# Performance work log

Measured on AMD Instinct MI355X. Metric: run time of the kernel, lower is better.

Reference implementation:

```python
import jax, jax.numpy as jnp
import numpy as np

N, E, B = 8000, 128000, 16
DIN, D, H, C, L = 16, 256, 8, 32, 6
MC, NT = 200, 8
NEG_SLOPE = 0.2


def layernorm(x, s, b):
    mu = jnp.mean(x, axis=-1, keepdims=True)
    var = jnp.mean(jnp.square(x - mu), axis=-1, keepdims=True)
    return (x - mu) * jax.lax.rsqrt(var + 1e-5) * s + b


def setup_inputs() -> dict:
    key = jax.random.key(0)
    ks = iter(jax.random.split(key, 64))
    rn = lambda shape, s=0.05: jax.random.normal(next(ks), shape, jnp.float32) * s
    inp = {}
    inp['x'] = jax.random.normal(next(ks), (N, DIN), jnp.float32)
    inp['edge_index'] = jax.random.randint(next(ks), (2, E), 0, N)
    inp['batch'] = jnp.sort(jax.random.randint(next(ks), (N,), 0, B))
    # node encoder: Linear(DIN,D) + LayerNorm
    inp['enc_W'] = rn((DIN, D)); inp['enc_b'] = jnp.zeros((D,), jnp.float32)
    inp['enc_ls'] = jnp.ones((D,), jnp.float32); inp['enc_lb'] = jnp.zeros((D,), jnp.float32)
    # GATv2 layers (stacked): lin_l, lin_r, att, output bias, post LayerNorm
    inp['Wl'] = rn((L, D, D)); inp['bl'] = jnp.zeros((L, D), jnp.float32)
    inp['Wr'] = rn((L, D, D)); inp['br'] = jnp.zeros((L, D), jnp.float32)
    inp['att'] = rn((L, H, C))
    inp['gb'] = jnp.zeros((L, D), jnp.float32)
    inp['gls'] = jnp.ones((L, D), jnp.float32); inp['glb'] = jnp.zeros((L, D), jnp.float32)
    # color head MLP: D -> D -> D//2 -> MC
    inp['cW1'] = rn((D, D)); inp['cb1'] = jnp.zeros((D,), jnp.float32)
    inp['cW2'] = rn((D, D // 2)); inp['cb2'] = jnp.zeros((D // 2,), jnp.float32)
    inp['cW3'] = rn((D // 2, MC)); inp['cb3'] = jnp.zeros((MC,), jnp.float32)
    # chromatic head: 2D -> D -> D//2 -> MC
    inp['chW1'] = rn((2 * D, D)); inp['chb1'] = jnp.zeros((D,), jnp.float32)
    inp['chW2'] = rn((D, D // 2)); inp['chb2'] = jnp.zeros((D // 2,), jnp.float32)
    inp['chW3'] = rn((D // 2, MC)); inp['chb3'] = jnp.zeros((MC,), jnp.float32)
    # type head: 2D -> 128 -> NT
    inp['tW1'] = rn((2 * D, 128)); inp['tb1'] = jnp.zeros((128,), jnp.float32)
    inp['tW2'] = rn((128, NT)); inp['tb2'] = jnp.zeros((NT,), jnp.float32)
    # difficulty head: 2D -> 64 -> 1, sigmoid * 100
    inp['dW1'] = rn((2 * D, 64)); inp['db1'] = jnp.zeros((64,), jnp.float32)
    inp['dW2'] = rn((64, 1)); inp['db2'] = jnp.zeros((1,), jnp.float32)
    return inp


def reference(x, edge_index, batch, enc_W, enc_b, enc_ls, enc_lb,
              Wl, bl, Wr, br, att, gb, gls, glb,
              cW1, cb1, cW2, cb2, cW3, cb3,
              chW1, chb1, chW2, chb2, chW3, chb3,
              tW1, tb1, tW2, tb2, dW1, db1, dW2, db2):
    n = x.shape[0]
    # node encoder (dropout = identity at inference)
    h = jax.nn.relu(layernorm(x @ enc_W + enc_b, enc_ls, enc_lb))
    # add self loops once (same for every layer)
    sl = jnp.arange(n)
    src = jnp.concatenate([edge_index[0], sl])  # message source j
    dst = jnp.concatenate([edge_index[1], sl])  # message target i
    for i in range(L):
        xl = (h @ Wl[i] + bl[i]).reshape(n, H, C)  # source transform
        xr = (h @ Wr[i] + br[i]).reshape(n, H, C)  # target transform
        # GATv2 attention: a^T LeakyReLU(xl_j + xr_i)
        e = jax.nn.leaky_relu(xl[src] + xr[dst], NEG_SLOPE)  # [E+N, H, C]
        logits = jnp.einsum('ehc,hc->eh', e, att[i])          # [E+N, H]
        # segment softmax over destination node (self-loops guarantee denom > 0)
        m = jax.ops.segment_max(logits, dst, num_segments=n)
        m = jnp.where(jnp.isfinite(m), m, 0.0)
        p = jnp.exp(logits - m[dst])
        denom = jax.ops.segment_sum(p, dst, num_segments=n)
        alpha = p / denom[dst]
        out = jax.ops.segment_sum(xl[src] * alpha[:, :, None], dst, num_segments=n)
        out = out.reshape(n, D) + gb[i]
        h_new = jax.nn.elu(layernorm(out, gls[i], glb[i]))
        h = h + h_new if i > 0 else h_new
    # per-node color logits
    z = jax.nn.relu(h @ cW1 + cb1)
    z = jax.nn.relu(z @ cW2 + cb2)
    node_colors = z @ cW3 + cb3
    # global mean/max pooling per graph
    cnt = jax.ops.segment_sum(jnp.ones((n,), h.dtype), batch, num_segments=B)
    mean_p = jax.ops.segment_sum(h, batch, num_segments=B) / jnp.maximum(cnt, 1.0)[:, None]
    max_p = jax.ops.segment_max(h, batch, num_segments=B)
    max_p = jnp.where(jnp.isfinite(max_p), max_p, 0.0)
    g = jnp.concatenate([mean_p, max_p], axis=1)  # [B, 2D]
    zc = jax.nn.relu(g @ chW1 + chb1)
    zc = jax.nn.relu(zc @ chW2 + chb2)
    chromatic_num = zc @ chW3 + chb3
    zt = jax.nn.relu(g @ tW1 + tb1)
    graph_type = zt @ tW2 + tb2
    zd = jax.nn.relu(g @ dW1 + db1)
    difficulty = jax.nn.sigmoid(zd @ dW2 + db2) * 100.0
    return (node_colors, chromatic_num, graph_type, difficulty)
```

## Files before the change

### kernel.cpp

```cpp
#include <hip/hip_runtime.h>
#include <hip/hip_bf16.h>

constexpr int DIN = 16;
constexpr int D   = 256;
constexpr int NH  = 8;
constexpr int NC  = 32;
constexpr int MC  = 200;
constexpr int NT  = 8;
constexpr int BG  = 16;
constexpr int NL  = 6;
constexpr float NEG = 0.2f;

typedef __attribute__((ext_vector_type(8))) short bfrag;
typedef __attribute__((ext_vector_type(4))) float f32x4;

__device__ inline unsigned short f2bf(float f) {
    unsigned int u = __float_as_uint(f);
    u += 0x7FFFu + ((u >> 16) & 1u);
    return (unsigned short)(u >> 16);
}
__device__ inline float bf2f(unsigned short u) {
    return __uint_as_float((unsigned int)u << 16);
}

__device__ inline float dot_ilp(const float* g, const float* __restrict__ W, int K, int ldw, int t) {
    float a0 = 0.f, a1 = 0.f, a2 = 0.f, a3 = 0.f;
    for (int k = 0; k < K; k += 4) {
        a0 = fmaf(g[k + 0], W[(k + 0) * ldw + t], a0);
        a1 = fmaf(g[k + 1], W[(k + 1) * ldw + t], a1);
        a2 = fmaf(g[k + 2], W[(k + 2) * ldw + t], a2);
        a3 = fmaf(g[k + 3], W[(k + 3) * ldw + t], a3);
    }
    return (a0 + a1) + (a2 + a3);
}


__device__ inline void enc_node(const float* x, const float* W, const float* b, const float* ls,
                                const float* lb, float* h, int n, int lane) {
    int c4 = lane * 4;
    float xs[DIN];
#pragma unroll
    for (int k = 0; k < DIN; k += 4) {
        float4 xv = *(const float4*)&x[n * DIN + k];
        xs[k] = xv.x; xs[k + 1] = xv.y; xs[k + 2] = xv.z; xs[k + 3] = xv.w;
    }
    float4 a = *(const float4*)&b[c4];
#pragma unroll
    for (int k = 0; k < DIN; k++) {
        float4 wv = *(const float4*)&W[k * D + c4];
        a.x = fmaf(xs[k], wv.x, a.x);
        a.y = fmaf(xs[k], wv.y, a.y);
        a.z = fmaf(xs[k], wv.z, a.z);
        a.w = fmaf(xs[k], wv.w, a.w);
    }
    float s = a.x + a.y + a.z + a.w;
#pragma unroll
    for (int msk = 1; msk <= 32; msk <<= 1) s += __shfl_xor(s, msk);
    float mu = s * (1.f / D);
    float4 dv = make_float4(a.x - mu, a.y - mu, a.z - mu, a.w - mu);
    float v2 = dv.x * dv.x + dv.y * dv.y + dv.z * dv.z + dv.w * dv.w;
#pragma unroll
    for (int msk = 1; msk <= 32; msk <<= 1) v2 += __shfl_xor(v2, msk);
    float rstd = rsqrtf(v2 * (1.f / D) + 1e-5f);
    float4 lsv = *(const float4*)&ls[c4];
    float4 lbv = *(const float4*)&lb[c4];
    float4 y = make_float4(fmaxf(dv.x * rstd * lsv.x + lbv.x, 0.f),
                           fmaxf(dv.y * rstd * lsv.y + lbv.y, 0.f),
                           fmaxf(dv.z * rstd * lsv.z + lbv.z, 0.f),
                           fmaxf(dv.w * rstd * lsv.w + lbv.w, 0.f));
    *(float4*)&h[(size_t)n * D + c4] = y;
}

__device__ inline float4 attn_compute(const unsigned short* xl, const unsigned short* xr,
                                      const int* row_ptr, const int* col, const float* att,
                                      const float* gb, const float* gls, const float* glb,
                                      const float* h, int layer, int n, int lane) {
    int c4 = lane * 4;
    ushort4 xr4 = *(const ushort4*)&xr[(size_t)n * D + c4];
    float4 xrv = make_float4(bf2f(xr4.x), bf2f(xr4.y), bf2f(xr4.z), bf2f(xr4.w));
    float4 av  = *(const float4*)&att[c4];
    int beg = row_ptr[n], end = row_ptr[n + 1];
    int deg = end - beg;
    int myc = col[beg + min(lane, deg - 1)];
    float l = 0.f;
    float4 acc = make_float4(0.f, 0.f, 0.f, 0.f);
    auto loadx = [&](int i) -> ushort4 {
        if (i < deg) {
            int s = (i < 64) ? __shfl(myc, i) : col[beg + i];
            return *(const ushort4*)&xl[(size_t)s * D + c4];
        }
        return make_ushort4(0, 0, 0, 0);
    };
    auto step = [&](ushort4 x4) {
        float4 xlv = make_float4(bf2f(x4.x), bf2f(x4.y), bf2f(x4.z), bf2f(x4.w));
        float sx = xlv.x + xrv.x; sx = sx > 0.f ? sx : NEG * sx;
        float sy = xlv.y + xrv.y; sy = sy > 0.f ? sy : NEG * sy;
        float sz = xlv.z + xrv.z; sz = sz > 0.f ? sz : NEG * sz;
        float sw = xlv.w + xrv.w; sw = sw > 0.f ? sw : NEG * sw;
        float z = av.x * sx + av.y * sy + av.z * sz + av.w * sw;
        z += __shfl_xor(z, 1); z += __shfl_xor(z, 2); z += __shfl_xor(z, 4);
        float p = __expf(z);
        l += p;
        acc.x = fmaf(p, xlv.x, acc.x);
        acc.y = fmaf(p, xlv.y, acc.y);
        acc.z = fmaf(p, xlv.z, acc.z);
        acc.w = fmaf(p, xlv.w, acc.w);
    };
    ushort4 b0 = loadx(0), b1 = loadx(1), b2 = loadx(2), b3 = loadx(3);
    int e = 0;
    for (; e + 4 <= deg; e += 4) {
        ushort4 n0 = loadx(e + 4), n1 = loadx(e + 5), n2 = loadx(e + 6), n3 = loadx(e + 7);
        step(b0); step(b1); step(b2); step(b3);
        b0 = n0; b1 = n1; b2 = n2; b3 = n3;
    }
    if (e + 0 < deg) step(b0);
    if (e + 1 < deg) step(b1);
    if (e + 2 < deg) step(b2);
    float4 gbv = *(const float4*)&gb[c4];
    float rl = 1.f / l;
    float4 o = make_float4(acc.x * rl + gbv.x, acc.y * rl + gbv.y,
                           acc.z * rl + gbv.z, acc.w * rl + gbv.w);
    float s = o.x + o.y + o.z + o.w;
#pragma unroll
    for (int msk = 1; msk <= 32; msk <<= 1) s += __shfl_xor(s, msk);
    float mu = s * (1.f / D);
    float4 dv = make_float4(o.x - mu, o.y - mu, o.z - mu, o.w - mu);
    float v2 = dv.x * dv.x + dv.y * dv.y + dv.z * dv.z + dv.w * dv.w;
#pragma unroll
    for (int msk = 1; msk <= 32; msk <<= 1) v2 += __shfl_xor(v2, msk);
    float rstd = rsqrtf(v2 * (1.f / D) + 1e-5f);
    float4 glsv = *(const float4*)&gls[c4];
    float4 glbv = *(const float4*)&glb[c4];
    float y0 = dv.x * rstd * glsv.x + glbv.x;
    float y1 = dv.y * rstd * glsv.y + glbv.y;
    float y2 = dv.z * rstd * glsv.z + glbv.z;
    float y3 = dv.w * rstd * glsv.w + glbv.w;
    y0 = y0 > 0.f ? y0 : expm1f(y0);
    y1 = y1 > 0.f ? y1 : expm1f(y1);
    y2 = y2 > 0.f ? y2 : expm1f(y2);
    y3 = y3 > 0.f ? y3 : expm1f(y3);
    float4 prev = make_float4(0.f, 0.f, 0.f, 0.f);
    if (layer > 0) prev = *(const float4*)&h[(size_t)n * D + c4];
    return make_float4(prev.x + y0, prev.y + y1, prev.z + y2, prev.w + y3);
}

__device__ inline void gemm_one_ct(const unsigned short (*As)[264],
                                   const unsigned short* WpL, const unsigned short* WpR,
                                   const float* bl, const float* br,
                                   unsigned short* xl, unsigned short* xr,
                                   int N, int nb, int ctg, int lane) {
    int m = lane & 15, q = lane >> 4;
    float bLv = bl[ctg * 16 + m];
    float bRv = br[ctg * 16 + m];
    f32x4 accL = (f32x4){bLv, bLv, bLv, bLv};
    f32x4 accR = (f32x4){bRv, bRv, bRv, bRv};
#pragma unroll
    for (int ks = 0; ks < 8; ks++) {
        bfrag af = *(const bfrag*)&As[m][ks * 32 + q * 8];
        size_t off = (((size_t)ctg * 8 + ks) * 64 + lane) * 8;
        bfrag bL = *(const bfrag*)&WpL[off];
        bfrag bR = *(const bfrag*)&WpR[off];
        accL = __builtin_amdgcn_mfma_f32_16x16x32_bf16(af, bL, accL, 0, 0, 0);
        accR = __builtin_amdgcn_mfma_f32_16x16x32_bf16(af, bR, accR, 0, 0, 0);
    }
    int colg = ctg * 16 + m;
#pragma unroll
    for (int reg = 0; reg < 4; reg++) {
        int row = nb + q * 4 + reg;
        if (row < N) {
            xl[(size_t)row * D + colg] = f2bf(accL[reg]);
            xr[(size_t)row * D + colg] = f2bf(accR[reg]);
        }
    }
}

__device__ inline void gemm_core(const unsigned short (*As)[264],
                                 const unsigned short* WpL, const unsigned short* WpR,
                                 const float* bl, const float* br,
                                 unsigned short* xl, unsigned short* xr, int N, int nb, int T) {
    int lane = T & 63, w = T >> 6;
#pragma unroll
    for (int ct = 0; ct < 4; ct++)
        gemm_one_ct(As, WpL, WpR, bl, br, xl, xr, N, nb, w * 4 + ct, lane);
}

__device__ inline void repack_attn_one(const float* Wl, const float* Wr, unsigned short* Wp, int tid) {
    int lane = tid & 63;
    int r1 = tid >> 6;
    int ks = r1 & 7;
    int r2 = r1 >> 3;
    int ct = r2 & 15;
    int mi = r2 >> 4;
    int layer = mi >> 1, mat = mi & 1;
    const float* W = (mat == 0 ? Wl : Wr) + (size_t)layer * D * D;
    int n = ct * 16 + (lane & 15);
    int kb = ks * 32 + (lane >> 4) * 8;
    size_t base = (((size_t)(mi * 16 + ct) * 8 + ks) * 64 + lane) * 8;
#pragma unroll
    for (int j = 0; j < 8; j++) Wp[base + j] = f2bf(W[(size_t)(kb + j) * D + n]);
}

__device__ inline void repack_gen_one(const float* W, unsigned short* Wp, int K, int NCOL, int nks, int tid) {
    int lane = tid & 63;
    int r = tid >> 6;
    int ks = r % nks;
    int ct = r / nks;
    int n = ct * 16 + (lane & 15);
    int kb = ks * 32 + (lane >> 4) * 8;
    size_t base = (((size_t)ct * nks + ks) * 64 + lane) * 8;
#pragma unroll
    for (int j = 0; j < 8; j++) {
        int k = kb + j;
        Wp[base + j] = (n < NCOL && k < K) ? f2bf(W[(size_t)k * NCOL + n]) : (unsigned short)0;
    }
}


__global__ __launch_bounds__(256) void fused_init_k(const float* __restrict__ x, const float* __restrict__ encW,
                                                    const float* __restrict__ encb, const float* __restrict__ encls,
                                                    const float* __restrict__ enclb, float* __restrict__ h, int N,
                                                    const int* __restrict__ dst, int* __restrict__ deg, int E,
                                                    const float* __restrict__ Wl, const float* __restrict__ Wr,
                                                    unsigned short* __restrict__ Wp,
                                                    const float* __restrict__ cW1, unsigned short* __restrict__ cW1p,
                                                    const float* __restrict__ cW2, unsigned short* __restrict__ cW2p,
                                                    const float* __restrict__ cW3, unsigned short* __restrict__ cW3p) {
    int gid = blockIdx.x * 256 + threadIdx.x;
    int lane = threadIdx.x & 63;
    int n = blockIdx.x * 4 + (threadIdx.x >> 6);
    if (n < N) enc_node(x, encW, encb, encls, enclb, h, n, lane);
    if (gid < E) atomicAdd(&deg[dst[gid]], 1);
    if (gid < NL * 2 * 16 * 8 * 64) repack_attn_one(Wl, Wr, Wp, gid);
    if (gid < 16 * 8 * 64) repack_gen_one(cW1, cW1p, D, D, 8, gid);
    if (gid < 8 * 8 * 64)  repack_gen_one(cW2, cW2p, D, 128, 8, gid);
    if (gid < 13 * 4 * 64) repack_gen_one(cW3, cW3p, 128, MC, 4, gid);
}

__global__ __launch_bounds__(1024) void scan_k(const int* __restrict__ deg, int* __restrict__ row_ptr,
                                               int* __restrict__ fill, int N) {
    __shared__ int sd[1024];
    int t = threadIdx.x;
    int chunk = (N + 1023) >> 10;
    int lo = t * chunk, hi = min(lo + chunk, N);
    int s = 0;
    for (int i = lo; i < hi; i++) s += deg[i] + 1;
    sd[t] = s;
    __syncthreads();
    for (int off = 1; off < 1024; off <<= 1) {
        int v = (t >= off) ? sd[t - off] : 0;
        __syncthreads();
        sd[t] += v;
        __syncthreads();
    }
    int run = (t > 0) ? sd[t - 1] : 0;
    for (int i = lo; i < hi; i++) {
        row_ptr[i] = run; fill[i] = run;
        run += deg[i] + 1;
    }
    if (t == 1023) row_ptr[N] = sd[1023];
}

__global__ __launch_bounds__(256) void scatter_gemm0_k(const int* __restrict__ src, const int* __restrict__ dst,
                                                       int* __restrict__ fill, int* __restrict__ col, int E, int N,
                                                       const float* __restrict__ h,
                                                       const unsigned short* __restrict__ WpL,
                                                       const unsigned short* __restrict__ WpR,
                                                       const float* __restrict__ bl, const float* __restrict__ br,
                                                       unsigned short* __restrict__ xl, unsigned short* __restrict__ xr) {
    __shared__ unsigned short As[16][264];
    int T = threadIdx.x;
    int tt = blockIdx.x;
    int ntiles = (N + 15) >> 4;
    if (tt < ntiles) {
        int nb = tt * 16;
#pragma unroll
        for (int r = 0; r < 16; r++) {
            int row = nb + r;
            float v = (row < N) ? h[(size_t)row * D + T] : 0.f;
            As[r][T] = f2bf(v);
        }
        __syncthreads();
        gemm_core(As, WpL, WpR, bl, br, xl, xr, N, nb, T);
    }
    for (int e = blockIdx.x * 256 + T; e < E + N; e += gridDim.x * 256) {
        if (e < E) {
            int p = atomicAdd(&fill[dst[e]], 1);
            col[p] = src[e];
        } else {
            int n = e - E;
            int p = atomicAdd(&fill[n], 1);
            col[p] = n;
        }
    }
}

__global__ __launch_bounds__(1024) void layer_k(const unsigned short* __restrict__ xl_in,
                                                const unsigned short* __restrict__ xr_in,
                                                const int* __restrict__ row_ptr, const int* __restrict__ col,
                                                const float* __restrict__ att, const float* __restrict__ gb,
                                                const float* __restrict__ gls, const float* __restrict__ glb,
                                                float* __restrict__ h, int layer, int N,
                                                const unsigned short* __restrict__ WpL,
                                                const unsigned short* __restrict__ WpR,
                                                const float* __restrict__ bl, const float* __restrict__ br,
                                                unsigned short* __restrict__ xl_out, unsigned short* __restrict__ xr_out) {
    __shared__ unsigned short As[16][264];
    int T = threadIdx.x;
    int lane = T & 63, wv = T >> 6;
    int nb = blockIdx.x * 16;
    int c4 = lane * 4;
    int n = nb + wv;
    if (n < N) {
        float4 r = attn_compute(xl_in, xr_in, row_ptr, col, att, gb, gls, glb, h, layer, n, lane);
        *(float4*)&h[(size_t)n * D + c4] = r;
        As[wv][c4 + 0] = f2bf(r.x);
        As[wv][c4 + 1] = f2bf(r.y);
        As[wv][c4 + 2] = f2bf(r.z);
        As[wv][c4 + 3] = f2bf(r.w);
    } else {
        As[wv][c4 + 0] = 0; As[wv][c4 + 1] = 0; As[wv][c4 + 2] = 0; As[wv][c4 + 3] = 0;
    }
    __syncthreads();
    gemm_one_ct((const unsigned short (*)[264])As, WpL, WpR, bl, br, xl_out, xr_out, N, nb, wv, lane);
}

__global__ __launch_bounds__(1024) void last_k(const unsigned short* __restrict__ xl_in,
                                               const unsigned short* __restrict__ xr_in,
                                               const int* __restrict__ row_ptr, const int* __restrict__ col,
                                               const float* __restrict__ att, const float* __restrict__ gb,
                                               const float* __restrict__ gls, const float* __restrict__ glb,
                                               float* __restrict__ h, int N,
                                               const unsigned short* __restrict__ W1p, const float* __restrict__ b1,
                                               const unsigned short* __restrict__ W2p, const float* __restrict__ b2,
                                               const unsigned short* __restrict__ W3p, const float* __restrict__ b3,
                                               float* __restrict__ out) {
    __shared__ unsigned short As[16][264];
    __shared__ unsigned short Zs[16][264];
    int T = threadIdx.x;
    int lane = T & 63, wv = T >> 6;
    int nb = blockIdx.x * 16;
    int c4 = lane * 4;
    int n = nb + wv;
    if (n < N) {
        float4 res = attn_compute(xl_in, xr_in, row_ptr, col, att, gb, gls, glb, h, NL - 1, n, lane);
        *(float4*)&h[(size_t)n * D + c4] = res;
        As[wv][c4 + 0] = f2bf(res.x);
        As[wv][c4 + 1] = f2bf(res.y);
        As[wv][c4 + 2] = f2bf(res.z);
        As[wv][c4 + 3] = f2bf(res.w);
    } else {
        As[wv][c4 + 0] = 0; As[wv][c4 + 1] = 0; As[wv][c4 + 2] = 0; As[wv][c4 + 3] = 0;
    }
    __syncthreads();
    int m = lane & 15, q = lane >> 4;
    {
        float bv = b1[wv * 16 + m];
        f32x4 acc = (f32x4){bv, bv, bv, bv};
#pragma unroll
        for (int ks = 0; ks < 8; ks++) {
            bfrag af = *(const bfrag*)&As[m][ks * 32 + q * 8];
            bfrag bf = *(const bfrag*)&W1p[(((size_t)wv * 8 + ks) * 64 + lane) * 8];
            acc = __builtin_amdgcn_mfma_f32_16x16x32_bf16(af, bf, acc, 0, 0, 0);
        }
        int colg = wv * 16 + m;
#pragma unroll
        for (int reg = 0; reg < 4; reg++)
            Zs[q * 4 + reg][colg] = f2bf(fmaxf(acc[reg], 0.f));
    }
    __syncthreads();
    if (wv < 8) {
        float bv = b2[wv * 16 + m];
        f32x4 acc = (f32x4){bv, bv, bv, bv};
#pragma unroll
        for (int ks = 0; ks < 8; ks++) {
            bfrag af = *(const bfrag*)&Zs[m][ks * 32 + q * 8];
            bfrag bf = *(const bfrag*)&W2p[(((size_t)wv * 8 + ks) * 64 + lane) * 8];
            acc = __builtin_amdgcn_mfma_f32_16x16x32_bf16(af, bf, acc, 0, 0, 0);
        }
        int colg = wv * 16 + m;
#pragma unroll
        for (int reg = 0; reg < 4; reg++)
            As[q * 4 + reg][colg] = f2bf(fmaxf(acc[reg], 0.f));
    }
    __syncthreads();
    if (wv < 13) {
        int colg = wv * 16 + m;
        float bv = (colg < MC) ? b3[colg] : 0.f;
        f32x4 acc = (f32x4){bv, bv, bv, bv};
#pragma unroll
        for (int ks = 0; ks < 4; ks++) {
            bfrag af = *(const bfrag*)&As[m][ks * 32 + q * 8];
            bfrag bf = *(const bfrag*)&W3p[(((size_t)wv * 4 + ks) * 64 + lane) * 8];
            acc = __builtin_amdgcn_mfma_f32_16x16x32_bf16(af, bf, acc, 0, 0, 0);
        }
#pragma unroll
        for (int reg = 0; reg < 4; reg++) {
            int row = nb + q * 4 + reg;
            if (row < N && colg < MC) out[(size_t)row * MC + colg] = acc[reg];
        }
    }
}

__global__ __launch_bounds__(1024) void poolheads_k(const float* __restrict__ h, const int* __restrict__ batch,
                                                    int N,
                                                    const float* __restrict__ chW1, const float* __restrict__ chb1,
                                                    const float* __restrict__ chW2, const float* __restrict__ chb2,
                                                    const float* __restrict__ chW3, const float* __restrict__ chb3,
                                                    const float* __restrict__ tW1, const float* __restrict__ tb1,
                                                    const float* __restrict__ tW2, const float* __restrict__ tb2,
                                                    const float* __restrict__ dW1, const float* __restrict__ db1,
                                                    const float* __restrict__ dW2, const float* __restrict__ db2,
                                                    float* __restrict__ out_ch, float* __restrict__ out_t,
                                                    float* __restrict__ out_d) {
    int b = blockIdx.x, t = threadIdx.x;
    int sl = t >> 8, c = t & 255;
    int lo = 0, hi = N;
    while (lo < hi) { int mid = (lo + hi) >> 1; if (batch[mid] < b) lo = mid + 1; else hi = mid; }
    int s0 = lo;
    lo = 0; hi = N;
    while (lo < hi) { int mid = (lo + hi) >> 1; if (batch[mid] < b + 1) lo = mid + 1; else hi = mid; }
    int s1 = lo;
    int len = s1 - s0;
    int chunk = (len + 3) >> 2;
    int n0 = s0 + sl * chunk;
    int n1 = min(n0 + chunk, s1);
    float sum = 0.f, mx = -3.0e38f;
    int n = n0;
    for (; n + 4 <= n1; n += 4) {
        float v0 = h[(size_t)(n + 0) * D + c];
        float v1 = h[(size_t)(n + 1) * D + c];
        float v2 = h[(size_t)(n + 2) * D + c];
        float v3 = h[(size_t)(n + 3) * D + c];
        sum += (v0 + v1) + (v2 + v3);
        mx = fmaxf(mx, fmaxf(fmaxf(v0, v1), fmaxf(v2, v3)));
    }
    for (; n < n1; n++) { float v = h[(size_t)n * D + c]; sum += v; mx = fmaxf(mx, v); }
    __shared__ float ps[4][256];
    __shared__ float pm[4][256];
    __shared__ float g[2 * D];
    __shared__ float z1[D];
    __shared__ float z2[128];
    ps[sl][c] = sum; pm[sl][c] = mx;
    __syncthreads();
    if (t < 256) {
        float s = (ps[0][t] + ps[1][t]) + (ps[2][t] + ps[3][t]);
        float m = fmaxf(fmaxf(pm[0][t], pm[1][t]), fmaxf(pm[2][t], pm[3][t]));
        g[t] = s / fmaxf((float)len, 1.f);
        g[D + t] = (len > 0) ? m : 0.f;
    }
    __syncthreads();
    if (t < 256) z1[t] = fmaxf(chb1[t] + dot_ilp(g, chW1, 2 * D, D, t), 0.f);
    __syncthreads();
    if (t < 128) z2[t] = fmaxf(chb2[t] + dot_ilp(z1, chW2, D, 128, t), 0.f);
    __syncthreads();
    if (t < MC) out_ch[b * MC + t] = chb3[t] + dot_ilp(z2, chW3, 128, MC, t);
    if (t < 128) z1[t] = fmaxf(tb1[t] + dot_ilp(g, tW1, 2 * D, 128, t), 0.f);
    __syncthreads();
    if (t < NT) out_t[b * NT + t] = tb2[t] + dot_ilp(z1, tW2, 128, NT, t);
    if (t < 64) z2[t] = fmaxf(db1[t] + dot_ilp(g, dW1, 2 * D, 64, t), 0.f);
    __syncthreads();
    if (t == 0) {
        float a = db2[0] + dot_ilp(z2, dW2, 64, 1, 0);
        out_d[b] = 100.f / (1.f + __expf(-a));
    }
}

extern "C" void kernel_launch(void* const* d_in, const int* in_sizes, int n_in,
                              void* d_out, int out_size, void* d_ws, size_t ws_size,
                              hipStream_t stream) {
    const float* x     = (const float*)d_in[0];
    const int*   ei    = (const int*)d_in[1];
    const int*   batch = (const int*)d_in[2];
    const float* encW  = (const float*)d_in[3];
    const float* encb  = (const float*)d_in[4];
    const float* encls = (const float*)d_in[5];
    const float* enclb = (const float*)d_in[6];
    const float* Wl    = (const float*)d_in[7];
    const float* bl    = (const float*)d_in[8];
    const float* Wr    = (const float*)d_in[9];
    const float* br    = (const float*)d_in[10];
    const float* att   = (const float*)d_in[11];
    const float* gb    = (const float*)d_in[12];
    const float* gls   = (const float*)d_in[13];
    const float* glb   = (const float*)d_in[14];
    const float* cW1   = (const float*)d_in[15];
    const float* cb1   = (const float*)d_in[16];
    const float* cW2   = (const float*)d_in[17];
    const float* cb2   = (const float*)d_in[18];
    const float* cW3   = (const float*)d_in[19];
    const float* cb3   = (const float*)d_in[20];
    const float* chW1  = (const float*)d_in[21];
    const float* chb1  = (const float*)d_in[22];
    const float* chW2  = (const float*)d_in[23];
    const float* chb2  = (const float*)d_in[24];
    const float* chW3  = (const float*)d_in[25];
    const float* chb3  = (const float*)d_in[26];
    const float* tW1   = (const float*)d_in[27];
    const float* tb1   = (const float*)d_in[28];
    const float* tW2   = (const float*)d_in[29];
    const float* tb2   = (const float*)d_in[30];
    const float* dW1   = (const float*)d_in[31];
    const float* db1   = (const float*)d_in[32];
    const float* dW2   = (const float*)d_in[33];
    const float* db2   = (const float*)d_in[34];

    const int N = in_sizes[0] / DIN;
    const int E = in_sizes[1] / 2;
    const int* esrc = ei;
    const int* edst = ei + E;

    char* p = (char*)d_ws;
    auto carve = [&](size_t bytes) { char* r = p; p += (bytes + 255) & ~(size_t)255; return r; };
    int*            row_ptr = (int*)carve((size_t)(N + 1) * 4);
    int*            fill    = (int*)carve((size_t)N * 4);
    int*            deg     = (int*)carve((size_t)N * 4);
    int*            col     = (int*)carve((size_t)(E + N) * 4);
    unsigned short* Wp      = (unsigned short*)carve((size_t)NL * 2 * 65536 * 2);
    unsigned short* cW1p    = (unsigned short*)carve((size_t)16 * 8 * 64 * 8 * 2);
    unsigned short* cW2p    = (unsigned short*)carve((size_t)8 * 8 * 64 * 8 * 2);
    unsigned short* cW3p    = (unsigned short*)carve((size_t)13 * 4 * 64 * 8 * 2);
    float*          h       = (float*)carve((size_t)N * D * 4);
    unsigned short* xlA     = (unsigned short*)carve((size_t)N * D * 2);
    unsigned short* xrA     = (unsigned short*)carve((size_t)N * D * 2);
    unsigned short* xlB     = (unsigned short*)carve((size_t)N * D * 2);
    unsigned short* xrB     = (unsigned short*)carve((size_t)N * D * 2);
    (void)ws_size; (void)n_in; (void)out_size;

    const int ntiles16 = (N + 15) / 16;
    const int sblocks  = max(ntiles16, (E + N + 255) / 256);
    const int fblocks  = max((N + 3) / 4, max((E + 255) / 256, 384));

    hipMemsetAsync(deg, 0, (size_t)N * 4, stream);
    fused_init_k<<<fblocks, 256, 0, stream>>>(x, encW, encb, encls, enclb, h, N,
                                              edst, deg, E, Wl, Wr, Wp,
                                              cW1, cW1p, cW2, cW2p, cW3, cW3p);
    scan_k<<<1, 1024, 0, stream>>>(deg, row_ptr, fill, N);
    scatter_gemm0_k<<<sblocks, 256, 0, stream>>>(esrc, edst, fill, col, E, N, h,
                                                 Wp + 0, Wp + (size_t)65536,
                                                 bl + 0, br + 0, xlA, xrA);
    for (int l = 0; l < NL - 1; l++) {
        const unsigned short* xin_l = (l & 1) ? xlB : xlA;
        const unsigned short* xin_r = (l & 1) ? xrB : xrA;
        unsigned short* xout_l = (l & 1) ? xlA : xlB;
        unsigned short* xout_r = (l & 1) ? xrA : xrB;
        layer_k<<<ntiles16, 1024, 0, stream>>>(xin_l, xin_r, row_ptr, col, att + l * NH * NC,
                                               gb + l * D, gls + l * D, glb + l * D, h, l, N,
                                               Wp + (size_t)((l + 1) * 2 + 0) * 65536,
                                               Wp + (size_t)((l + 1) * 2 + 1) * 65536,
                                               bl + (l + 1) * D, br + (l + 1) * D, xout_l, xout_r);
    }
    float* out = (float*)d_out;
    last_k<<<ntiles16, 1024, 0, stream>>>(xlB, xrB, row_ptr, col, att + (NL - 1) * NH * NC,
                                          gb + (NL - 1) * D, gls + (NL - 1) * D, glb + (NL - 1) * D, h, N,
                                          cW1p, cb1, cW2p, cb2, cW3p, cb3, out);
    poolheads_k<<<BG, 1024, 0, stream>>>(h, batch, N, chW1, chb1, chW2, chb2, chW3, chb3,
                                         tW1, tb1, tW2, tb2, dW1, db1, dW2, db2,
                                         out + (size_t)N * MC,
                                         out + (size_t)N * MC + BG * MC,
                                         out + (size_t)N * MC + BG * MC + BG * NT);
}
```

Before: 447.8 us.

## Split pooling and graph heads into separate wider-grid kernels

After: 425.3 us. 1.05x faster.

```diff
diff --git a/kernel.cpp b/kernel.cpp
--- a/kernel.cpp
+++ b/kernel.cpp
@@ -9,6 +9,7 @@
 constexpr int NT  = 8;
 constexpr int BG  = 16;
 constexpr int NL  = 6;
+constexpr int PS  = 16;
 constexpr float NEG = 0.2f;
 
 typedef __attribute__((ext_vector_type(8))) short bfrag;
@@ -401,19 +402,12 @@
     }
 }
 
-__global__ __launch_bounds__(1024) void poolheads_k(const float* __restrict__ h, const int* __restrict__ batch,
-                                                    int N,
-                                                    const float* __restrict__ chW1, const float* __restrict__ chb1,
-                                                    const float* __restrict__ chW2, const float* __restrict__ chb2,
-                                                    const float* __restrict__ chW3, const float* __restrict__ chb3,
-                                                    const float* __restrict__ tW1, const float* __restrict__ tb1,
-                                                    const float* __restrict__ tW2, const float* __restrict__ tb2,
-                                                    const float* __restrict__ dW1, const float* __restrict__ db1,
-                                                    const float* __restrict__ dW2, const float* __restrict__ db2,
-                                                    float* __restrict__ out_ch, float* __restrict__ out_t,
-                                                    float* __restrict__ out_d) {
-    int b = blockIdx.x, t = threadIdx.x;
-    int sl = t >> 8, c = t & 255;
+__global__ __launch_bounds__(256) void pool_k(const float* __restrict__ h, const int* __restrict__ batch,
+                                              float* __restrict__ psum, float* __restrict__ pmax,
+                                              int* __restrict__ cnt, int N) {
+    int b = blockIdx.x;
+    int sl = blockIdx.y;
+    int c = threadIdx.x;
     int lo = 0, hi = N;
     while (lo < hi) { int mid = (lo + hi) >> 1; if (batch[mid] < b) lo = mid + 1; else hi = mid; }
     int s0 = lo;
@@ -421,47 +415,63 @@
     while (lo < hi) { int mid = (lo + hi) >> 1; if (batch[mid] < b + 1) lo = mid + 1; else hi = mid; }
     int s1 = lo;
     int len = s1 - s0;
-    int chunk = (len + 3) >> 2;
+    int chunk = (len + PS - 1) / PS;
     int n0 = s0 + sl * chunk;
     int n1 = min(n0 + chunk, s1);
     float sum = 0.f, mx = -3.0e38f;
-    int n = n0;
-    for (; n + 4 <= n1; n += 4) {
-        float v0 = h[(size_t)(n + 0) * D + c];
-        float v1 = h[(size_t)(n + 1) * D + c];
-        float v2 = h[(size_t)(n + 2) * D + c];
-        float v3 = h[(size_t)(n + 3) * D + c];
-        sum += (v0 + v1) + (v2 + v3);
-        mx = fmaxf(mx, fmaxf(fmaxf(v0, v1), fmaxf(v2, v3)));
-    }
-    for (; n < n1; n++) { float v = h[(size_t)n * D + c]; sum += v; mx = fmaxf(mx, v); }
-    __shared__ float ps[4][256];
-    __shared__ float pm[4][256];
+    for (int n = n0; n < n1; n++) {
+        float v = h[(size_t)n * D + c];
+        sum += v;
+        mx = fmaxf(mx, v);
+    }
+    psum[(size_t)(b * PS + sl) * D + c] = sum;
+    pmax[(size_t)(b * PS + sl) * D + c] = mx;
+    if (c == 0 && sl == 0) cnt[b] = len;
+}
+
+__global__ __launch_bounds__(256) void heads_k(const float* __restrict__ psum, const float* __restrict__ pmax,
+                                               const int* __restrict__ cnt,
+                                               const float* __restrict__ chW1, const float* __restrict__ chb1,
+                                               const float* __restrict__ chW2, const float* __restrict__ chb2,
+                                               const float* __restrict__ chW3, const float* __restrict__ chb3,
+                                               const float* __restrict__ tW1, const float* __restrict__ tb1,
+                                               const float* __restrict__ tW2, const float* __restrict__ tb2,
+                                               const float* __restrict__ dW1, const float* __restrict__ db1,
+                                               const float* __restrict__ dW2, const float* __restrict__ db2,
+                                               float* __restrict__ out_ch, float* __restrict__ out_t,
+                                               float* __restrict__ out_d) {
+    int b = blockIdx.x, sec = blockIdx.y, t = threadIdx.x;
     __shared__ float g[2 * D];
     __shared__ float z1[D];
     __shared__ float z2[128];
-    ps[sl][c] = sum; pm[sl][c] = mx;
+    float sum = 0.f, mx = -3.0e38f;
+#pragma unroll
+    for (int sl = 0; sl < PS; sl++) {
+        sum += psum[(size_t)(b * PS + sl) * D + t];
+        mx = fmaxf(mx, pmax[(size_t)(b * PS + sl) * D + t]);
+    }
+    int cn = cnt[b];
+    float c = fmaxf((float)cn, 1.f);
+    g[t] = sum / c;
+    g[D + t] = (cn > 0) ? mx : 0.f;
     __syncthreads();
-    if (t < 256) {
-        float s = (ps[0][t] + ps[1][t]) + (ps[2][t] + ps[3][t]);
-        float m = fmaxf(fmaxf(pm[0][t], pm[1][t]), fmaxf(pm[2][t], pm[3][t]));
-        g[t] = s / fmaxf((float)len, 1.f);
-        g[D + t] = (len > 0) ? m : 0.f;
-    }
-    __syncthreads();
-    if (t < 256) z1[t] = fmaxf(chb1[t] + dot_ilp(g, chW1, 2 * D, D, t), 0.f);
-    __syncthreads();
-    if (t < 128) z2[t] = fmaxf(chb2[t] + dot_ilp(z1, chW2, D, 128, t), 0.f);
-    __syncthreads();
-    if (t < MC) out_ch[b * MC + t] = chb3[t] + dot_ilp(z2, chW3, 128, MC, t);
-    if (t < 128) z1[t] = fmaxf(tb1[t] + dot_ilp(g, tW1, 2 * D, 128, t), 0.f);
-    __syncthreads();
-    if (t < NT) out_t[b * NT + t] = tb2[t] + dot_ilp(z1, tW2, 128, NT, t);
-    if (t < 64) z2[t] = fmaxf(db1[t] + dot_ilp(g, dW1, 2 * D, 64, t), 0.f);
-    __syncthreads();
-    if (t == 0) {
-        float a = db2[0] + dot_ilp(z2, dW2, 64, 1, 0);
-        out_d[b] = 100.f / (1.f + __expf(-a));
+    if (sec == 0) {
+        z1[t] = fmaxf(chb1[t] + dot_ilp(g, chW1, 2 * D, D, t), 0.f);
+        __syncthreads();
+        if (t < 128) z2[t] = fmaxf(chb2[t] + dot_ilp(z1, chW2, D, 128, t), 0.f);
+        __syncthreads();
+        if (t < MC) out_ch[b * MC + t] = chb3[t] + dot_ilp(z2, chW3, 128, MC, t);
+    } else if (sec == 1) {
+        if (t < 128) z1[t] = fmaxf(tb1[t] + dot_ilp(g, tW1, 2 * D, 128, t), 0.f);
+        __syncthreads();
+        if (t < NT) out_t[b * NT + t] = tb2[t] + dot_ilp(z1, tW2, 128, NT, t);
+    } else {
+        if (t < 64) z1[t] = fmaxf(db1[t] + dot_ilp(g, dW1, 2 * D, 64, t), 0.f);
+        __syncthreads();
+        if (t == 0) {
+            float a = db2[0] + dot_ilp(z1, dW2, 64, 1, 0);
+            out_d[b] = 100.f / (1.f + __expf(-a));
+        }
     }
 }
 
@@ -514,6 +524,9 @@
     int*            row_ptr = (int*)carve((size_t)(N + 1) * 4);
     int*            fill    = (int*)carve((size_t)N * 4);
     int*            deg     = (int*)carve((size_t)N * 4);
+    int*            cnt     = (int*)carve((size_t)BG * 4);
+    float*          psum    = (float*)carve((size_t)BG * PS * D * 4);
+    float*          pmax    = (float*)carve((size_t)BG * PS * D * 4);
     int*            col     = (int*)carve((size_t)(E + N) * 4);
     unsigned short* Wp      = (unsigned short*)carve((size_t)NL * 2 * 65536 * 2);
     unsigned short* cW1p    = (unsigned short*)carve((size_t)16 * 8 * 64 * 8 * 2);
@@ -553,9 +566,10 @@
     last_k<<<ntiles16, 1024, 0, stream>>>(xlB, xrB, row_ptr, col, att + (NL - 1) * NH * NC,
                                           gb + (NL - 1) * D, gls + (NL - 1) * D, glb + (NL - 1) * D, h, N,
                                           cW1p, cb1, cW2p, cb2, cW3p, cb3, out);
-    poolheads_k<<<BG, 1024, 0, stream>>>(h, batch, N, chW1, chb1, chW2, chb2, chW3, chb3,
-                                         tW1, tb1, tW2, tb2, dW1, db1, dW2, db2,
-                                         out + (size_t)N * MC,
-                                         out + (size_t)N * MC + BG * MC,
-                                         out + (size_t)N * MC + BG * MC + BG * NT);
-}
+    pool_k<<<dim3(BG, PS), 256, 0, stream>>>(h, batch, psum, pmax, cnt, N);
+    heads_k<<<dim3(BG, 3), 256, 0, stream>>>(psum, pmax, cnt, chW1, chb1, chW2, chb2, chW3, chb3,
+                                             tW1, tb1, tW2, tb2, dW1, db1, dW2, db2,
+                                             out + (size_t)N * MC,
+                                             out + (size_t)N * MC + BG * MC,
+                                             out + (size_t)N * MC + BG * MC + BG * NT);
+}
```
